# Optimization experiments

Measured on AMD Instinct MI355X. Metric: run time of the kernel, lower is better.

The kernel has to match this reference:

```python
import jax, jax.numpy as jnp
import numpy as np

# dims
B, N, D, F, L = 512, 128, 256, 16, 3
EPS = 1e-7
MAX_NORM = 1.0 - 1e-5  # PoincareBall proj boundary (c = 1.0)


def _proj(x):
    """Project points into the open Poincare ball (c=1)."""
    n = jnp.maximum(jnp.linalg.norm(x, axis=-1, keepdims=True), EPS)
    scale = jnp.where(n > MAX_NORM, MAX_NORM / n, 1.0)
    return x * scale


def _expmap0(u):
    """Exponential map at the origin, c=1: tanh(||u||) * u / ||u||."""
    n = jnp.maximum(jnp.linalg.norm(u, axis=-1, keepdims=True), EPS)
    return jnp.tanh(n) * u / n


def _logmap0(x):
    """Log map at the origin, c=1: artanh(||x||) * x / ||x||."""
    n = jnp.maximum(jnp.linalg.norm(x, axis=-1, keepdims=True), EPS)
    return jnp.arctanh(jnp.minimum(n, MAX_NORM)) * x / n


def setup_inputs() -> dict:
    key = jax.random.key(0)
    ks = jax.random.split(key, 6)
    # manifold input points: small tangent vectors -> inside the ball
    x = 0.01 * jax.random.normal(ks[0], (B, N, D), dtype=jnp.float32)
    adj = jax.random.uniform(ks[1], (B, N, N), dtype=jnp.float32)
    node_mask = jnp.ones((B, N, 1), dtype=jnp.float32)
    # per-layer HGC linear weights (tangent-space linear), hidden_dim -> hidden_dim
    Ws = jax.random.normal(ks[2], (L, D, D), dtype=jnp.float32) / np.sqrt(D)
    bs = jnp.zeros((L, D), dtype=jnp.float32)
    # final masked linear: hidden_dim -> max_feat_num
    Wout = jax.random.normal(ks[3], (D, F), dtype=jnp.float32) / np.sqrt(D)
    bout = jnp.zeros((F,), dtype=jnp.float32)
    return {"x": x, "adj": adj, "node_mask": node_mask,
            "Ws": Ws, "bs": bs, "Wout": Wout, "bout": bout}


def reference(x, adj, node_mask, Ws, bs, Wout, bout):
    # HGCN decoder: stack of hyperbolic graph-conv layers on the Poincare ball
    # (logmap0 -> tangent linear -> adjacency aggregation -> ReLU -> expmap0),
    # then logmap0 and a masked linear head.
    h = _proj(x)
    for i in range(L):
        t = _logmap0(h)                                  # [B,N,D] tangent at origin
        t = t @ Ws[i] + bs[i]                            # tangent linear
        t = jnp.einsum('bij,bjd->bid', adj, t)           # sum aggregation, norm factor 1
        t = jax.nn.relu(t)                               # activation in tangent space
        h = _proj(_expmap0(t))                           # back to the manifold
    out_tan = _logmap0(h)                                # manifold.logmap0 decode
    type_pred = (out_tan @ Wout + bout) * node_mask      # [B,N,F]
    return type_pred
```

## Files before the change

### kernel.cpp

```cpp
#include <hip/hip_runtime.h>
#include <hip/hip_bf16.h>
#include <math.h>


typedef _Float16 f16;
typedef f16 f16x8 __attribute__((ext_vector_type(8)));
typedef f16 f16x4 __attribute__((ext_vector_type(4)));
typedef f16 f16x2 __attribute__((ext_vector_type(2)));
typedef __fp16 fp16x2_cv __attribute__((ext_vector_type(2)));
typedef float f32x4 __attribute__((ext_vector_type(4)));
typedef float f32x16 __attribute__((ext_vector_type(16)));

#define NB 512
#define NN 128
#define ND 256
#define NF 16
#define NL 3

#define SDT 264
#define SDV 136

#define EPSV   1e-7f
#define MAXN   0.99999f
#define ATHMAX 6.1030340f

__device__ __forceinline__ f16x4 pack4(float a, float b, float c, float d) {
    fp16x2_cv lo = __builtin_amdgcn_cvt_pkrtz(a, b);
    fp16x2_cv hi = __builtin_amdgcn_cvt_pkrtz(c, d);
    f16x2 lo2, hi2;
    __builtin_memcpy(&lo2, &lo, sizeof(lo2));
    __builtin_memcpy(&hi2, &hi, sizeof(hi2));
    return __builtin_shufflevector(lo2, hi2, 0, 1, 2, 3);
}

__global__ void prep_kernel(const float* __restrict__ Ws,
                            const float* __restrict__ Wout,
                            f16* __restrict__ Wt, f16* __restrict__ WoutT) {
    int idx = blockIdx.x * 256 + threadIdx.x;
    if (idx < NL * ND * ND) {
        int l = idx / (ND * ND);
        int r = idx % (ND * ND);
        int n = r >> 8;
        int k = r & 255;
        Wt[idx] = (f16)Ws[l * ND * ND + k * ND + n];
    }
    if (idx < NF * ND) {
        int f = idx >> 8;
        int k = idx & 255;
        WoutT[idx] = (f16)Wout[k * NF + f];
    }
}

__global__ __launch_bounds__(1024, 4)
void hgcn_kernel(const float* __restrict__ x,
                 const float* __restrict__ adj,
                 const float* __restrict__ node_mask,
                 const f16*  __restrict__ Wt,
                 const float* __restrict__ bs,
                 const f16*  __restrict__ WoutT,
                 const float* __restrict__ bout,
                 float* __restrict__ out) {
    __shared__ __align__(16) f16 sT[NN * SDT];
    __shared__ __align__(16) f16 sV[ND * SDV];
    __shared__ __align__(16) float sRed[NN * 4];

    const int b    = blockIdx.x;
    const int tid  = threadIdx.x;
    const int wave = tid >> 6;
    const int lane = tid & 63;
    const int l31  = lane & 31;
    const int hi   = lane >> 5;
    const int lg   = lane >> 4;
    const int lc   = lane & 15;

    const int nr2 = wave >> 2;
    const int ic  = wave & 3;

    const f32x16 fzero16 = {0.f};

    f16x8 adjf[8];
    {
        const float* adjb = adj + (size_t)b * NN * NN;
        #pragma unroll
        for (int ks = 0; ks < 8; ++ks) {
            const float4* ap = (const float4*)(adjb + (ic * 32 + l31) * NN + ks * 16 + hi * 8);
            float4 alo = ap[0], ahi = ap[1];
            f16x4 l4 = pack4(alo.x, alo.y, alo.z, alo.w);
            f16x4 h4 = pack4(ahi.x, ahi.y, ahi.z, ahi.w);
            adjf[ks] = __builtin_shufflevector(l4, h4, 0, 1, 2, 3, 4, 5, 6, 7);
        }
    }

    const f16* wbase = Wt + (wave * 16 + lc) * ND + lg * 8;
    f16x8 wreg[8];
    #pragma unroll
    for (int k = 0; k < 8; ++k)
        wreg[k] = *(const f16x8*)(wbase + k * 32);

    {
        const float4* xb = (const float4*)(x + (size_t)b * NN * ND);
        #pragma unroll
        for (int r = 0; r < 8; ++r) {
            int row = wave * 8 + r;
            float4 v = xb[row * 64 + lane];
            float ssq = v.x * v.x + v.y * v.y + v.z * v.z + v.w * v.w;
            #pragma unroll
            for (int d = 1; d < 64; d <<= 1) ssq += __shfl_xor(ssq, d);
            float norm = sqrtf(ssq);
            float sc1 = (norm > MAXN) ? (MAXN / norm) : 1.0f;
            float hn  = fmaxf(norm * sc1, EPSV);
            float aa  = fminf(hn, MAXN);
            float ath = 0.5f * __logf((1.0f + aa) / (1.0f - aa));
            float s   = sc1 * ath / hn;
            *(f16x4*)&sT[row * SDT + lane * 4] =
                pack4(v.x * s, v.y * s, v.z * s, v.w * s);
        }
    }
    __syncthreads();

    for (int layer = 0; layer < NL; ++layer) {
        const float bias = bs[layer * ND + wave * 16 + lc];

        f32x4 acc_a[8];
        #pragma unroll
        for (int t = 0; t < 8; ++t) acc_a[t] = (f32x4){0.f, 0.f, 0.f, 0.f};

        #pragma unroll
        for (int ks = 0; ks < 8; ++ks) {
            f16x8 bfr = wreg[ks];
            #pragma unroll
            for (int mt = 0; mt < 8; ++mt) {
                f16x8 afr = *(const f16x8*)&sT[(mt * 16 + lc) * SDT + ks * 32 + lg * 8];
                acc_a[mt] = __builtin_amdgcn_mfma_f32_16x16x32_f16(afr, bfr, acc_a[mt], 0, 0, 0);
            }
        }

        if (layer + 1 < NL) {
            const f16* wn = wbase + (layer + 1) * ND * ND;
            #pragma unroll
            for (int k = 0; k < 8; ++k)
                wreg[k] = *(const f16x8*)(wn + k * 32);
        } else {
            const f16* wn = WoutT + lc * ND + lg * 8;
            #pragma unroll
            for (int k = 0; k < 8; ++k)
                wreg[k] = *(const f16x8*)(wn + k * 32);
        }

        #pragma unroll
        for (int mt = 0; mt < 8; ++mt) {
            int n  = wave * 16 + lc;
            int m0 = mt * 16 + lg * 4;
            *(f16x4*)&sV[n * SDV + m0] =
                pack4(acc_a[mt][0] + bias, acc_a[mt][1] + bias,
                      acc_a[mt][2] + bias, acc_a[mt][3] + bias);
        }
        __syncthreads();

        f32x16 acc_b0 = fzero16, acc_b1 = fzero16;
        #pragma unroll
        for (int ks = 0; ks < 8; ++ks) {
            f16x8 a0 = *(const f16x8*)&sV[((2 * nr2 + 0) * 32 + l31) * SDV + ks * 16 + hi * 8];
            f16x8 a1 = *(const f16x8*)&sV[((2 * nr2 + 1) * 32 + l31) * SDV + ks * 16 + hi * 8];
            acc_b0 = __builtin_amdgcn_mfma_f32_32x32x16_f16(a0, adjf[ks], acc_b0, 0, 0, 0);
            acc_b1 = __builtin_amdgcn_mfma_f32_32x32x16_f16(a1, adjf[ks], acc_b1, 0, 0, 0);
        }

        float ssq = 0.f;
        #pragma unroll
        for (int r = 0; r < 16; ++r) {
            float v0 = fmaxf(acc_b0[r], 0.0f);
            float v1 = fmaxf(acc_b1[r], 0.0f);
            acc_b0[r] = v0;
            acc_b1[r] = v1;
            ssq += v0 * v0 + v1 * v1;
        }
        ssq += __shfl_xor(ssq, 32);
        if (lane < 32) sRed[(ic * 32 + l31) * 4 + nr2] = ssq;
        __syncthreads();

        f32x4 p = *(const f32x4*)&sRed[(ic * 32 + l31) * 4];
        float tot = p[0] + p[1] + p[2] + p[3];
        float nu = sqrtf(tot);
        float scale = (nu > ATHMAX) ? (ATHMAX / nu) : 1.0f;

        {
            int i = ic * 32 + l31;
            #pragma unroll
            for (int g = 0; g < 4; ++g) {
                int n0 = (2 * nr2 + 0) * 32 + 8 * g + 4 * hi;
                int n1 = (2 * nr2 + 1) * 32 + 8 * g + 4 * hi;
                *(f16x4*)&sT[i * SDT + n0] =
                    pack4(acc_b0[4 * g + 0] * scale, acc_b0[4 * g + 1] * scale,
                          acc_b0[4 * g + 2] * scale, acc_b0[4 * g + 3] * scale);
                *(f16x4*)&sT[i * SDT + n1] =
                    pack4(acc_b1[4 * g + 0] * scale, acc_b1[4 * g + 1] * scale,
                          acc_b1[4 * g + 2] * scale, acc_b1[4 * g + 3] * scale);
            }
        }
        __syncthreads();
    }

    if (wave < 8) {
        f32x4 acc = {0.f, 0.f, 0.f, 0.f};
        #pragma unroll
        for (int ks = 0; ks < 8; ++ks) {
            f16x8 afr = *(const f16x8*)&sT[(wave * 16 + lc) * SDT + ks * 32 + lg * 8];
            acc = __builtin_amdgcn_mfma_f32_16x16x32_f16(afr, wreg[ks], acc, 0, 0, 0);
        }
        #pragma unroll
        for (int r = 0; r < 4; ++r) {
            int row = wave * 16 + lg * 4 + r;
            float mask = node_mask[b * NN + row];
            out[((size_t)b * NN + row) * NF + lc] = (acc[r] + bout[lc]) * mask;
        }
    }
}

extern "C" void kernel_launch(void* const* d_in, const int* in_sizes, int n_in,
                              void* d_out, int out_size, void* d_ws, size_t ws_size,
                              hipStream_t stream) {
    const float* x    = (const float*)d_in[0];
    const float* adj  = (const float*)d_in[1];
    const float* mask = (const float*)d_in[2];
    const float* Ws   = (const float*)d_in[3];
    const float* bsp  = (const float*)d_in[4];
    const float* Wout = (const float*)d_in[5];
    const float* bout = (const float*)d_in[6];

    f16* Wt    = (f16*)d_ws;
    f16* WoutT = Wt + NL * ND * ND;

    prep_kernel<<<768, 256, 0, stream>>>(Ws, Wout, Wt, WoutT);
    hgcn_kernel<<<NB, 1024, 0, stream>>>(x, adj, mask, Wt, bsp, WoutT, bout,
                                         (float*)d_out);
}
```

Before: 88.37 us.

## Retile tangent GEMM to 64x32 per wave and reload adjacency each layer

The first GEMM is retiled so each wave computes a 64-row by 32-column block, holding two weight fragments instead of one 16-column strip over all 128 rows. This halves the LDS A-fragment reads per MFMA. The adjacency fragments are no longer kept in registers across layers; they are reloaded from global memory and converted each layer to cut register pressure. Weight prefetch for the next layer moves after the aggregation GEMM. The cost is repeated global adjacency reads and conversions, three times per block instead of once.

```diff
diff --git a/kernel.cpp b/kernel.cpp
--- a/kernel.cpp
+++ b/kernel.cpp
@@ -73,29 +73,24 @@
     const int lg   = lane >> 4;
     const int lc   = lane & 15;
 
+    const int mh  = wave >> 3;
+    const int nc8 = wave & 7;
     const int nr2 = wave >> 2;
     const int ic  = wave & 3;
 
     const f32x16 fzero16 = {0.f};
-
-    f16x8 adjf[8];
+    const float* adjb = adj + (size_t)b * NN * NN;
+
+    f16x8 bf[2][8];
     {
-        const float* adjb = adj + (size_t)b * NN * NN;
-        #pragma unroll
-        for (int ks = 0; ks < 8; ++ks) {
-            const float4* ap = (const float4*)(adjb + (ic * 32 + l31) * NN + ks * 16 + hi * 8);
-            float4 alo = ap[0], ahi = ap[1];
-            f16x4 l4 = pack4(alo.x, alo.y, alo.z, alo.w);
-            f16x4 h4 = pack4(ahi.x, ahi.y, ahi.z, ahi.w);
-            adjf[ks] = __builtin_shufflevector(l4, h4, 0, 1, 2, 3, 4, 5, 6, 7);
-        }
-    }
-
-    const f16* wbase = Wt + (wave * 16 + lc) * ND + lg * 8;
-    f16x8 wreg[8];
-    #pragma unroll
-    for (int k = 0; k < 8; ++k)
-        wreg[k] = *(const f16x8*)(wbase + k * 32);
+        const f16* w0 = Wt + (nc8 * 32 + 0 * 16 + lc) * ND + lg * 8;
+        const f16* w1 = Wt + (nc8 * 32 + 1 * 16 + lc) * ND + lg * 8;
+        #pragma unroll
+        for (int ks = 0; ks < 8; ++ks) {
+            bf[0][ks] = *(const f16x8*)(w0 + ks * 32);
+            bf[1][ks] = *(const f16x8*)(w1 + ks * 32);
+        }
+    }
 
     {
         const float4* xb = (const float4*)(x + (size_t)b * NN * ND);
@@ -118,42 +113,47 @@
     }
     __syncthreads();
 
+    f16x8 adjf[8];
+
     for (int layer = 0; layer < NL; ++layer) {
-        const float bias = bs[layer * ND + wave * 16 + lc];
-
-        f32x4 acc_a[8];
-        #pragma unroll
-        for (int t = 0; t < 8; ++t) acc_a[t] = (f32x4){0.f, 0.f, 0.f, 0.f};
-
-        #pragma unroll
-        for (int ks = 0; ks < 8; ++ks) {
-            f16x8 bfr = wreg[ks];
-            #pragma unroll
-            for (int mt = 0; mt < 8; ++mt) {
-                f16x8 afr = *(const f16x8*)&sT[(mt * 16 + lc) * SDT + ks * 32 + lg * 8];
-                acc_a[mt] = __builtin_amdgcn_mfma_f32_16x16x32_f16(afr, bfr, acc_a[mt], 0, 0, 0);
-            }
-        }
-
-        if (layer + 1 < NL) {
-            const f16* wn = wbase + (layer + 1) * ND * ND;
-            #pragma unroll
-            for (int k = 0; k < 8; ++k)
-                wreg[k] = *(const f16x8*)(wn + k * 32);
-        } else {
-            const f16* wn = WoutT + lc * ND + lg * 8;
-            #pragma unroll
-            for (int k = 0; k < 8; ++k)
-                wreg[k] = *(const f16x8*)(wn + k * 32);
-        }
-
-        #pragma unroll
-        for (int mt = 0; mt < 8; ++mt) {
-            int n  = wave * 16 + lc;
-            int m0 = mt * 16 + lg * 4;
-            *(f16x4*)&sV[n * SDV + m0] =
-                pack4(acc_a[mt][0] + bias, acc_a[mt][1] + bias,
-                      acc_a[mt][2] + bias, acc_a[mt][3] + bias);
+        f32x4 acc_a[4][2];
+        #pragma unroll
+        for (int mt = 0; mt < 4; ++mt)
+            #pragma unroll
+            for (int nt = 0; nt < 2; ++nt)
+                acc_a[mt][nt] = (f32x4){0.f, 0.f, 0.f, 0.f};
+
+        #pragma unroll
+        for (int ks = 0; ks < 8; ++ks) {
+            #pragma unroll
+            for (int mt = 0; mt < 4; ++mt) {
+                int row = mh * 64 + mt * 16 + lc;
+                f16x8 afr = *(const f16x8*)&sT[row * SDT + ks * 32 + lg * 8];
+                acc_a[mt][0] = __builtin_amdgcn_mfma_f32_16x16x32_f16(afr, bf[0][ks], acc_a[mt][0], 0, 0, 0);
+                acc_a[mt][1] = __builtin_amdgcn_mfma_f32_16x16x32_f16(afr, bf[1][ks], acc_a[mt][1], 0, 0, 0);
+            }
+        }
+
+        #pragma unroll
+        for (int ks = 0; ks < 8; ++ks) {
+            const float4* ap = (const float4*)(adjb + (ic * 32 + l31) * NN + ks * 16 + hi * 8);
+            float4 alo = ap[0], ahi = ap[1];
+            f16x4 l4 = pack4(alo.x, alo.y, alo.z, alo.w);
+            f16x4 h4 = pack4(ahi.x, ahi.y, ahi.z, ahi.w);
+            adjf[ks] = __builtin_shufflevector(l4, h4, 0, 1, 2, 3, 4, 5, 6, 7);
+        }
+
+        #pragma unroll
+        for (int nt = 0; nt < 2; ++nt) {
+            int n = nc8 * 32 + nt * 16 + lc;
+            float bias = bs[layer * ND + n];
+            #pragma unroll
+            for (int mt = 0; mt < 4; ++mt) {
+                int m0 = mh * 64 + mt * 16 + lg * 4;
+                *(f16x4*)&sV[n * SDV + m0] =
+                    pack4(acc_a[mt][nt][0] + bias, acc_a[mt][nt][1] + bias,
+                          acc_a[mt][nt][2] + bias, acc_a[mt][nt][3] + bias);
+            }
         }
         __syncthreads();
 
@@ -164,6 +164,21 @@
             f16x8 a1 = *(const f16x8*)&sV[((2 * nr2 + 1) * 32 + l31) * SDV + ks * 16 + hi * 8];
             acc_b0 = __builtin_amdgcn_mfma_f32_32x32x16_f16(a0, adjf[ks], acc_b0, 0, 0, 0);
             acc_b1 = __builtin_amdgcn_mfma_f32_32x32x16_f16(a1, adjf[ks], acc_b1, 0, 0, 0);
+        }
+
+        if (layer + 1 < NL) {
+            const f16* w0 = Wt + (layer + 1) * ND * ND + (nc8 * 32 + 0 * 16 + lc) * ND + lg * 8;
+            const f16* w1 = Wt + (layer + 1) * ND * ND + (nc8 * 32 + 1 * 16 + lc) * ND + lg * 8;
+            #pragma unroll
+            for (int ks = 0; ks < 8; ++ks) {
+                bf[0][ks] = *(const f16x8*)(w0 + ks * 32);
+                bf[1][ks] = *(const f16x8*)(w1 + ks * 32);
+            }
+        } else {
+            const f16* wh = WoutT + lc * ND + lg * 8;
+            #pragma unroll
+            for (int ks = 0; ks < 8; ++ks)
+                bf[0][ks] = *(const f16x8*)(wh + ks * 32);
         }
 
         float ssq = 0.f;
@@ -206,7 +221,7 @@
         #pragma unroll
         for (int ks = 0; ks < 8; ++ks) {
             f16x8 afr = *(const f16x8*)&sT[(wave * 16 + lc) * SDT + ks * 32 + lg * 8];
-            acc = __builtin_amdgcn_mfma_f32_16x16x32_f16(afr, wreg[ks], acc, 0, 0, 0);
+            acc = __builtin_amdgcn_mfma_f32_16x16x32_f16(afr, bf[0][ks], acc, 0, 0, 0);
         }
         #pragma unroll
         for (int r = 0; r < 4; ++r) {
```

Measured after the change: 123.5 us. +39.8%, slower.
